# Optimization experiments

Hardware: AMD Instinct MI355X
Metric: run time of the kernel (lower is better)

## Reference

```python
import jax, jax.numpy as jnp
import numpy as np

B, T, C = 2, 8192, 1024
H, BS, LW = 16, 64, 128          # num_heads, block_size, local_window_size
D = C // H                        # head_dim = 64
W = BS + LW                       # max window length per block = 192
NB = T // BS                      # number of blocks


def setup_inputs() -> dict:
    key = jax.random.key(0)
    ks = jax.random.split(key, 11)
    s = 1.0 / np.sqrt(C)          # small init so softmax is not saturated
    return {
        'query': jax.random.normal(ks[0], (B, T, C), jnp.float32),
        'key':   jax.random.normal(ks[1], (B, T, C), jnp.float32),
        'value': jax.random.normal(ks[2], (B, T, C), jnp.float32),
        'Wq': jax.random.normal(ks[3], (C, C), jnp.float32) * s,
        'bq': jax.random.normal(ks[4], (C,), jnp.float32) * s,
        'Wk': jax.random.normal(ks[5], (C, C), jnp.float32) * s,
        'bk': jax.random.normal(ks[6], (C,), jnp.float32) * s,
        'Wv': jax.random.normal(ks[7], (C, C), jnp.float32) * s,
        'bv': jax.random.normal(ks[8], (C,), jnp.float32) * s,
        'Wo': jax.random.normal(ks[9], (C, C), jnp.float32) * s,
        'bo': jax.random.normal(ks[10], (C,), jnp.float32) * s,
    }


def reference(query, key, value, Wq, bq, Wk, bk, Wv, bv, Wo, bo):
    # projections -> (B, H, T, D)
    def proj(x, Wt, bt):
        return (x @ Wt.T + bt).reshape(B, T, H, D).transpose(0, 2, 1, 3)

    scale = jnp.asarray(D, query.dtype) ** -0.5
    q = proj(query, Wq, bq) * scale
    k = proj(key, Wk, bk)
    v = proj(value, Wv, bv)

    # per-block window indices: block i attends to [i - LW//2, i + BS + LW//2)
    starts = jnp.arange(NB) * BS                              # (NB,)
    idx = starts[:, None] + jnp.arange(-LW // 2, BS + LW // 2)  # (NB, W)
    valid = (idx >= 0) & (idx < T)                            # (NB, W)
    cidx = jnp.clip(idx, 0, T - 1)

    q_blk = q.reshape(B, H, NB, BS, D)
    k_win = k[:, :, cidx, :]                                  # (B, H, NB, W, D)
    v_win = v[:, :, cidx, :]

    scores = jnp.einsum('bhnqd,bhnkd->bhnqk', q_blk, k_win).astype(jnp.float32)
    scores = jnp.where(valid[None, None, :, None, :], scores, -jnp.inf)
    probs = jax.nn.softmax(scores, axis=-1).astype(q.dtype)

    out = jnp.einsum('bhnqk,bhnkd->bhnqd', probs, v_win)      # (B, H, NB, BS, D)
    out = out.reshape(B, H, T, D).transpose(0, 2, 1, 3).reshape(B, T, C)
    return out @ Wo.T + bo
```

## Files before the change

### kernel.cpp

```cpp
#include <hip/hip_runtime.h>
#include <hip/hip_bf16.h>
#include <type_traits>

#define BATCH 2
#define SEQ   8192
#define CH    1024
#define NH    16
#define BLK   64
#define WIN   192
#define NBL   128
#define DH    64
#define MR    (BATCH*SEQ)

typedef __bf16 bf16x8 __attribute__((ext_vector_type(8)));
typedef float  f32x4  __attribute__((ext_vector_type(4)));

__device__ __forceinline__ f32x4 zero4() {
    f32x4 z; z[0]=0.f; z[1]=0.f; z[2]=0.f; z[3]=0.f; return z;
}

union Pack8 { __hip_bfloat16 h[8]; uint4 u; };

typedef const __attribute__((address_space(1))) unsigned int* gas_ptr;
typedef       __attribute__((address_space(3))) unsigned int* las_ptr;

__device__ __forceinline__ void gload_lds16(const __hip_bfloat16* g, __hip_bfloat16* l) {
    __builtin_amdgcn_global_load_lds((gas_ptr)(const void*)g, (las_ptr)(void*)l, 16, 0, 0);
}

__device__ __forceinline__ int xcd_swz(int bid, int nwg) {
    return (bid & 7) * (nwg >> 3) + (bid >> 3);
}

__global__ __launch_bounds__(256) void pack_bf16(
    const float* __restrict__ src, __hip_bfloat16* __restrict__ dst, int n8)
{
    int i = blockIdx.x * 256 + threadIdx.x;
    if (i >= n8) return;
    const float4* s = reinterpret_cast<const float4*>(src);
    float4 a = s[2 * i], b = s[2 * i + 1];
    Pack8 p;
    p.h[0] = __float2bfloat16(a.x); p.h[1] = __float2bfloat16(a.y);
    p.h[2] = __float2bfloat16(a.z); p.h[3] = __float2bfloat16(a.w);
    p.h[4] = __float2bfloat16(b.x); p.h[5] = __float2bfloat16(b.y);
    p.h[6] = __float2bfloat16(b.z); p.h[7] = __float2bfloat16(b.w);
    reinterpret_cast<uint4*>(dst)[i] = p.u;
}


__device__ __forceinline__ void stage_half(
    const __hip_bfloat16* __restrict__ g, int goff,
    __hip_bfloat16* sm, int loff, int tid)
{
    gload_lds16(g + goff,            sm + loff + tid * 8);
    gload_lds16(g + goff + 128 * CH, sm + loff + (tid + 512) * 8);
}

#define SB0 __builtin_amdgcn_sched_barrier(0)
#define LGKM0 do { asm volatile("s_waitcnt lgkmcnt(0)" ::: "memory"); \
                   __builtin_amdgcn_sched_barrier(0); } while (0)
#define VMCNT(n) do { asm volatile("s_waitcnt vmcnt(" #n ")" ::: "memory"); \
                      __builtin_amdgcn_sched_barrier(0); } while (0)

template<int MH, bool RB>
__device__ __forceinline__ void phase_reads(
    const __hip_bfloat16* Ak, const __hip_bfloat16* Bk,
    int aoff, int boff, bf16x8 (&af)[4], bf16x8 (&bfk)[4])
{
    if constexpr (RB) {
        #pragma unroll
        for (int j = 0; j < 4; ++j)
            bfk[j] = *reinterpret_cast<const bf16x8*>(Bk + boff + j * 512);
    }
    #pragma unroll
    for (int i = 0; i < 4; ++i)
        af[i] = *reinterpret_cast<const bf16x8*>(Ak + aoff + (MH * 4 + i) * 512);
}

template<int MH>
__device__ __forceinline__ void phase_mfma16(
    const bf16x8 (&af)[4], const bf16x8 (&bfk)[4], f32x4 (&acc)[8][4])
{
    __builtin_amdgcn_s_setprio(1);
    #pragma unroll
    for (int i = 0; i < 4; ++i)
        #pragma unroll
        for (int j = 0; j < 4; ++j)
            acc[MH * 4 + i][j] = __builtin_amdgcn_mfma_f32_16x16x32_bf16(
                af[i], bfk[j], acc[MH * 4 + i][j], 0, 0, 0);
    __builtin_amdgcn_s_setprio(0);
}

template<typename OT>
__device__ __forceinline__ void gemm_body256(
    const __hip_bfloat16* __restrict__ A, const __hip_bfloat16* __restrict__ Wb,
    const float* __restrict__ bias, OT* __restrict__ out, float alpha,
    int m0, int n0, __hip_bfloat16* sm)
{
    const int tid  = threadIdx.x;
    const int wid  = tid >> 6;
    const int lane = tid & 63;
    const int quad = lane >> 4;
    const int l16  = lane & 15;
    const int wr   = wid >> 2, wc = wid & 3;

    const int r0 = tid >> 2;
    const int s0 = (tid & 3) ^ ((tid >> 3) & 3);
    const int offA0 = (m0 + r0) * CH + s0 * 8;
    const int offB0 = (n0 + r0) * CH + s0 * 8;

    const int cq   = quad ^ ((l16 >> 1) & 3);
    const int aoff = ((wr * 128 + l16) * 4 + cq) * 8;
    const int boff = ((wc * 64  + l16) * 4 + cq) * 8;

    f32x4 acc[8][4];
    #pragma unroll
    for (int i = 0; i < 8; ++i)
        #pragma unroll
        for (int j = 0; j < 4; ++j) acc[i][j] = zero4();

    stage_half(A,  offA0,      sm, 0,             tid);
    stage_half(Wb, offB0,      sm, 32768,         tid);
    stage_half(A,  offA0 + 32, sm, 8192,          tid);
    stage_half(Wb, offB0 + 32, sm, 32768 + 8192,  tid);
    VMCNT(4);
    __builtin_amdgcn_s_barrier();
    SB0;

    bf16x8 af[4], bfk[4];

    #pragma unroll 1
    for (int t = 0; t < 15; ++t) {
        const int cur = t & 1, nb = cur ^ 1;
        const int kn  = (t + 1) * 64;
        const __hip_bfloat16* As_ = sm + cur * 16384;
        const __hip_bfloat16* Bs_ = sm + 32768 + cur * 16384;

        phase_reads<0, true>(As_, Bs_, aoff, boff, af, bfk);
        stage_half(A, offA0 + kn, sm, nb * 16384, tid);
        SB0;
        __builtin_amdgcn_s_barrier();
        LGKM0;
        phase_mfma16<0>(af, bfk, acc);
        __builtin_amdgcn_s_barrier();

        phase_reads<1, false>(As_, Bs_, aoff, boff, af, bfk);
        stage_half(Wb, offB0 + kn, sm, 32768 + nb * 16384, tid);
        SB0;
        __builtin_amdgcn_s_barrier();
        LGKM0;
        phase_mfma16<1>(af, bfk, acc);
        VMCNT(4);
        __builtin_amdgcn_s_barrier();

        phase_reads<0, true>(As_ + 8192, Bs_ + 8192, aoff, boff, af, bfk);
        stage_half(A, offA0 + kn + 32, sm, nb * 16384 + 8192, tid);
        SB0;
        __builtin_amdgcn_s_barrier();
        LGKM0;
        phase_mfma16<0>(af, bfk, acc);
        __builtin_amdgcn_s_barrier();

        phase_reads<1, false>(As_ + 8192, Bs_ + 8192, aoff, boff, af, bfk);
        stage_half(Wb, offB0 + kn + 32, sm, 32768 + nb * 16384 + 8192, tid);
        SB0;
        __builtin_amdgcn_s_barrier();
        LGKM0;
        phase_mfma16<1>(af, bfk, acc);
        VMCNT(4);
        __builtin_amdgcn_s_barrier();
    }

    {
        const __hip_bfloat16* As_ = sm + 16384;
        const __hip_bfloat16* Bs_ = sm + 32768 + 16384;

        phase_reads<0, true>(As_, Bs_, aoff, boff, af, bfk);
        SB0;
        __builtin_amdgcn_s_barrier();
        LGKM0;
        phase_mfma16<0>(af, bfk, acc);
        __builtin_amdgcn_s_barrier();

        phase_reads<1, false>(As_, Bs_, aoff, boff, af, bfk);
        SB0;
        __builtin_amdgcn_s_barrier();
        LGKM0;
        phase_mfma16<1>(af, bfk, acc);
        VMCNT(0);
        __builtin_amdgcn_s_barrier();

        phase_reads<0, true>(As_ + 8192, Bs_ + 8192, aoff, boff, af, bfk);
        SB0;
        __builtin_amdgcn_s_barrier();
        LGKM0;
        phase_mfma16<0>(af, bfk, acc);
        __builtin_amdgcn_s_barrier();

        phase_reads<1, false>(As_ + 8192, Bs_ + 8192, aoff, boff, af, bfk);
        SB0;
        __builtin_amdgcn_s_barrier();
        LGKM0;
        phase_mfma16<1>(af, bfk, acc);
    }

    #pragma unroll
    for (int j = 0; j < 4; ++j) {
        const int col = n0 + wc * 64 + j * 16 + l16;
        const float bv = bias[col];
        #pragma unroll
        for (int i = 0; i < 8; ++i) {
            #pragma unroll
            for (int r = 0; r < 4; ++r) {
                const int row = m0 + wr * 128 + i * 16 + quad * 4 + r;
                float v = alpha * (acc[i][j][r] + bv);
                if constexpr (std::is_same<OT, float>::value)
                    out[(size_t)row * CH + col] = v;
                else
                    out[(size_t)row * CH + col] = __float2bfloat16(v);
            }
        }
    }
}

__device__ __forceinline__ void gemm_tile256(int& m0, int& n0) {
    int bid = blockIdx.y * 4 + blockIdx.x;
    int swz = (bid & 7) * 32 + (bid >> 3);
    m0 = (swz >> 2) * 256;
    n0 = (swz & 3) * 256;
}

__global__ __launch_bounds__(512, 2) void gemm_qk256(
    const __hip_bfloat16* __restrict__ A0, const __hip_bfloat16* __restrict__ W0,
    const float* __restrict__ b0, __hip_bfloat16* __restrict__ o0, float alpha0,
    const __hip_bfloat16* __restrict__ A1, const __hip_bfloat16* __restrict__ W1,
    const float* __restrict__ b1, __hip_bfloat16* __restrict__ o1)
{
    __shared__ alignas(16) __hip_bfloat16 sm[65536];
    int m0, n0; gemm_tile256(m0, n0);
    if (blockIdx.z == 0)
        gemm_body256<__hip_bfloat16>(A0, W0, b0, o0, alpha0, m0, n0, sm);
    else
        gemm_body256<__hip_bfloat16>(A1, W1, b1, o1, 1.0f, m0, n0, sm);
}

template<typename OT>
__global__ __launch_bounds__(512, 2) void gemm_one256(
    const __hip_bfloat16* __restrict__ A, const __hip_bfloat16* __restrict__ Wb,
    const float* __restrict__ bias, OT* __restrict__ out)
{
    __shared__ alignas(16) __hip_bfloat16 sm[65536];
    int m0, n0; gemm_tile256(m0, n0);
    gemm_body256<OT>(A, Wb, bias, out, 1.0f, m0, n0, sm);
}

__global__ __launch_bounds__(256) void attn_kernel(
    const __hip_bfloat16* __restrict__ qg,
    const __hip_bfloat16* __restrict__ kg,
    const __hip_bfloat16* __restrict__ vg,
    __hip_bfloat16* __restrict__ ctx)
{
    __shared__ alignas(16) char smem[62464];
    auto qs = reinterpret_cast<__hip_bfloat16(*)[72]>(smem);
    auto ks = reinterpret_cast<__hip_bfloat16(*)[72]>(smem + 9216);
    auto vt = reinterpret_cast<__hip_bfloat16(*)[200]>(smem + 36864);
    auto ps = reinterpret_cast<__hip_bfloat16(*)[200]>(smem);

    const int blk = xcd_swz(blockIdx.x, BATCH * NH * NBL);
    const int n = blk & (NBL - 1);
    const int h = (blk >> 7) & (NH - 1);
    const int b = blk >> 11;
    const int t0  = n * BLK;
    const int kst = t0 - 64;
    const int tid = threadIdx.x;
    const size_t baseBH = (size_t)b * SEQ * CH + (size_t)h * DH;

    #pragma unroll
    for (int it = 0; it < 2; it++) {
        int c = tid + it * 256;
        int row = c >> 3, seg = c & 7;
        *reinterpret_cast<uint4*>(&qs[row][seg * 8]) =
            *reinterpret_cast<const uint4*>(qg + baseBH + (size_t)(t0 + row) * CH + seg * 8);
    }
    #pragma unroll
    for (int it = 0; it < 6; it++) {
        int c = tid + it * 256;
        int row = c >> 3, seg = c & 7;
        int tr = kst + row; tr = tr < 0 ? 0 : (tr >= SEQ ? SEQ - 1 : tr);
        *reinterpret_cast<uint4*>(&ks[row][seg * 8]) =
            *reinterpret_cast<const uint4*>(kg + baseBH + (size_t)tr * CH + seg * 8);
    }
    #pragma unroll
    for (int it = 0; it < 6; it++) {
        int c = tid + it * 256;
        int j = c % WIN, seg = c / WIN;
        int tr = kst + j; tr = tr < 0 ? 0 : (tr >= SEQ ? SEQ - 1 : tr);
        Pack8 p;
        p.u = *reinterpret_cast<const uint4*>(vg + baseBH + (size_t)tr * CH + seg * 8);
        #pragma unroll
        for (int e = 0; e < 8; e++) vt[seg * 8 + e][j] = p.h[e];
    }
    __syncthreads();

    const int wid = tid >> 6, lane = tid & 63, quad = lane >> 4, l16 = lane & 15;

    f32x4 sc[12];
    #pragma unroll
    for (int j = 0; j < 12; j++) sc[j] = zero4();
    #pragma unroll
    for (int kk = 0; kk < 2; kk++) {
        bf16x8 aq = *reinterpret_cast<const bf16x8*>(&qs[wid * 16 + l16][kk * 32 + quad * 8]);
        #pragma unroll
        for (int j = 0; j < 12; j++) {
            bf16x8 bk = *reinterpret_cast<const bf16x8*>(&ks[j * 16 + l16][kk * 32 + quad * 8]);
            sc[j] = __builtin_amdgcn_mfma_f32_16x16x32_bf16(aq, bk, sc[j], 0, 0, 0);
        }
    }
    __syncthreads();

    #pragma unroll
    for (int r = 0; r < 4; r++) {
        float s[12];
        float mx = -3.0e38f;
        #pragma unroll
        for (int j = 0; j < 12; j++) {
            int col = j * 16 + l16;
            int tr = kst + col;
            bool valid = (tr >= 0) && (tr < SEQ);
            s[j] = valid ? sc[j][r] : -3.0e38f;
            mx = fmaxf(mx, s[j]);
        }
        #pragma unroll
        for (int o = 1; o < 16; o <<= 1) mx = fmaxf(mx, __shfl_xor(mx, o, 64));
        float sum = 0.f;
        #pragma unroll
        for (int j = 0; j < 12; j++) {
            float e = __expf(s[j] - mx);
            s[j] = e;
            sum += e;
        }
        #pragma unroll
        for (int o = 1; o < 16; o <<= 1) sum += __shfl_xor(sum, o, 64);
        const float inv = 1.f / sum;
        const int row = wid * 16 + quad * 4 + r;
        #pragma unroll
        for (int j = 0; j < 12; j++)
            ps[row][j * 16 + l16] = __float2bfloat16(s[j] * inv);
    }
    __syncthreads();

    f32x4 oa[4];
    #pragma unroll
    for (int j = 0; j < 4; j++) oa[j] = zero4();
    #pragma unroll
    for (int kk = 0; kk < 6; kk++) {
        bf16x8 ap = *reinterpret_cast<const bf16x8*>(&ps[wid * 16 + l16][kk * 32 + quad * 8]);
        #pragma unroll
        for (int j = 0; j < 4; j++) {
            bf16x8 bv = *reinterpret_cast<const bf16x8*>(&vt[j * 16 + l16][kk * 32 + quad * 8]);
            oa[j] = __builtin_amdgcn_mfma_f32_16x16x32_bf16(ap, bv, oa[j], 0, 0, 0);
        }
    }
    #pragma unroll
    for (int j = 0; j < 4; j++) {
        const int d = j * 16 + l16;
        #pragma unroll
        for (int r = 0; r < 4; r++) {
            const int i = wid * 16 + quad * 4 + r;
            ctx[baseBH + (size_t)(t0 + i) * CH + d] = __float2bfloat16(oa[j][r]);
        }
    }
}

extern "C" void kernel_launch(void* const* d_in, const int* in_sizes, int n_in,
                              void* d_out, int out_size, void* d_ws, size_t ws_size,
                              hipStream_t stream)
{
    const float* query = (const float*)d_in[0];
    const float* key_i = (const float*)d_in[1];
    const float* value = (const float*)d_in[2];
    const float* Wq = (const float*)d_in[3];
    const float* bq = (const float*)d_in[4];
    const float* Wk = (const float*)d_in[5];
    const float* bk = (const float*)d_in[6];
    const float* Wv = (const float*)d_in[7];
    const float* bv = (const float*)d_in[8];
    const float* Wo = (const float*)d_in[9];
    const float* bo = (const float*)d_in[10];
    float* out = (float*)d_out;

    const size_t NELEM = (size_t)MR * CH;
    const size_t WELEM = (size_t)CH * CH;

    __hip_bfloat16* S0 = (__hip_bfloat16*)d_ws;
    __hip_bfloat16* S1 = S0 + NELEM;
    __hip_bfloat16* S2 = S1 + NELEM;
    __hip_bfloat16* S3 = S2 + NELEM;
    __hip_bfloat16* wqb = S3;
    __hip_bfloat16* wkb = S3 + WELEM;
    __hip_bfloat16* wvb = S3 + 2 * WELEM;
    __hip_bfloat16* wob = S3 + 3 * WELEM;

    __hip_bfloat16* xq = (__hip_bfloat16*)d_out;
    __hip_bfloat16* xk = xq + NELEM;
    __hip_bfloat16* vb = (__hip_bfloat16*)d_out;
    __hip_bfloat16* qb = S1;
    __hip_bfloat16* kb = S2;
    __hip_bfloat16* cb = S0;

    const int nA8 = (int)(NELEM / 8);
    const int nW8 = (int)(WELEM / 8);

    pack_bf16<<<nA8 / 256, 256, 0, stream>>>(query, xq, nA8);
    pack_bf16<<<nA8 / 256, 256, 0, stream>>>(key_i, xk, nA8);
    pack_bf16<<<nA8 / 256, 256, 0, stream>>>(value, S0, nA8);
    pack_bf16<<<nW8 / 256, 256, 0, stream>>>(Wq, wqb, nW8);
    pack_bf16<<<nW8 / 256, 256, 0, stream>>>(Wk, wkb, nW8);
    pack_bf16<<<nW8 / 256, 256, 0, stream>>>(Wv, wvb, nW8);
    pack_bf16<<<nW8 / 256, 256, 0, stream>>>(Wo, wob, nW8);

    dim3 ggrid(CH / 256, MR / 256);
    dim3 qkgrid(CH / 256, MR / 256, 2);

    gemm_qk256<<<qkgrid, 512, 0, stream>>>(xq, wqb, bq, qb, 0.125f,
                                           xk, wkb, bk, kb);
    gemm_one256<__hip_bfloat16><<<ggrid, 512, 0, stream>>>(S0, wvb, bv, vb);

    attn_kernel<<<BATCH * NH * NBL, 256, 0, stream>>>(qb, kb, vb, cb);

    gemm_one256<float><<<ggrid, 512, 0, stream>>>(cb, wob, bo, out);
}
```

Measured before the change: 448.8 us.

## Fuse bf16 pack launches and load attention Q directly into registers

Replaces seven separate fp32-to-bf16 pack launches with one pack_all kernel that routes each block to its source tensor by block index, removing launch overhead and tail gaps between the launches. In the attention kernel, Q fragments now go straight from global memory into MFMA operand registers instead of through LDS. This shrinks shared memory from about 61 KB to 52 KB, and the launch bound is raised to request 3 blocks per CU. The risks are uncoalesced per-lane Q loads and register pressure from the occupancy hint.

```diff
diff --git a/kernel.cpp b/kernel.cpp
--- a/kernel.cpp
+++ b/kernel.cpp
@@ -32,11 +32,33 @@
     return (bid & 7) * (nwg >> 3) + (bid >> 3);
 }
 
-__global__ __launch_bounds__(256) void pack_bf16(
-    const float* __restrict__ src, __hip_bfloat16* __restrict__ dst, int n8)
-{
-    int i = blockIdx.x * 256 + threadIdx.x;
-    if (i >= n8) return;
+__global__ __launch_bounds__(256) void pack_all(
+    const float* __restrict__ q,  const float* __restrict__ k,
+    const float* __restrict__ v,
+    const float* __restrict__ wq, const float* __restrict__ wk,
+    const float* __restrict__ wv, const float* __restrict__ wo,
+    __hip_bfloat16* __restrict__ xq, __hip_bfloat16* __restrict__ xk,
+    __hip_bfloat16* __restrict__ xv,
+    __hip_bfloat16* __restrict__ wqb, __hip_bfloat16* __restrict__ wkb,
+    __hip_bfloat16* __restrict__ wvb, __hip_bfloat16* __restrict__ wob)
+{
+    const int NA8B = (MR * CH / 8) / 256;
+    const int NW8B = (CH * CH / 8) / 256;
+    int bid = blockIdx.x;
+    const float* src;
+    __hip_bfloat16* dst;
+    int rel;
+    if (bid < 3 * NA8B) {
+        int t = bid / NA8B; rel = bid - t * NA8B;
+        src = (t == 0) ? q : (t == 1) ? k : v;
+        dst = (t == 0) ? xq : (t == 1) ? xk : xv;
+    } else {
+        int b2 = bid - 3 * NA8B;
+        int t = b2 / NW8B; rel = b2 - t * NW8B;
+        src = (t == 0) ? wq : (t == 1) ? wk : (t == 2) ? wv : wo;
+        dst = (t == 0) ? wqb : (t == 1) ? wkb : (t == 2) ? wvb : wob;
+    }
+    int i = rel * 256 + threadIdx.x;
     const float4* s = reinterpret_cast<const float4*>(src);
     float4 a = s[2 * i], b = s[2 * i + 1];
     Pack8 p;
@@ -254,16 +276,15 @@
     gemm_body256<OT>(A, Wb, bias, out, 1.0f, m0, n0, sm);
 }
 
-__global__ __launch_bounds__(256) void attn_kernel(
+__global__ __launch_bounds__(256, 3) void attn_kernel(
     const __hip_bfloat16* __restrict__ qg,
     const __hip_bfloat16* __restrict__ kg,
     const __hip_bfloat16* __restrict__ vg,
     __hip_bfloat16* __restrict__ ctx)
 {
-    __shared__ alignas(16) char smem[62464];
-    auto qs = reinterpret_cast<__hip_bfloat16(*)[72]>(smem);
-    auto ks = reinterpret_cast<__hip_bfloat16(*)[72]>(smem + 9216);
-    auto vt = reinterpret_cast<__hip_bfloat16(*)[200]>(smem + 36864);
+    __shared__ alignas(16) char smem[53248];
+    auto ks = reinterpret_cast<__hip_bfloat16(*)[72]>(smem);
+    auto vt = reinterpret_cast<__hip_bfloat16(*)[200]>(smem + 27648);
     auto ps = reinterpret_cast<__hip_bfloat16(*)[200]>(smem);
 
     const int blk = xcd_swz(blockIdx.x, BATCH * NH * NBL);
@@ -275,13 +296,12 @@
     const int tid = threadIdx.x;
     const size_t baseBH = (size_t)b * SEQ * CH + (size_t)h * DH;
 
-    #pragma unroll
-    for (int it = 0; it < 2; it++) {
-        int c = tid + it * 256;
-        int row = c >> 3, seg = c & 7;
-        *reinterpret_cast<uint4*>(&qs[row][seg * 8]) =
-            *reinterpret_cast<const uint4*>(qg + baseBH + (size_t)(t0 + row) * CH + seg * 8);
-    }
+    const int wid = tid >> 6, lane = tid & 63, quad = lane >> 4, l16 = lane & 15;
+
+    const __hip_bfloat16* qrow = qg + baseBH + (size_t)(t0 + wid * 16 + l16) * CH + quad * 8;
+    bf16x8 aq0 = *reinterpret_cast<const bf16x8*>(qrow);
+    bf16x8 aq1 = *reinterpret_cast<const bf16x8*>(qrow + 32);
+
     #pragma unroll
     for (int it = 0; it < 6; it++) {
         int c = tid + it * 256;
@@ -302,19 +322,15 @@
     }
     __syncthreads();
 
-    const int wid = tid >> 6, lane = tid & 63, quad = lane >> 4, l16 = lane & 15;
-
     f32x4 sc[12];
     #pragma unroll
     for (int j = 0; j < 12; j++) sc[j] = zero4();
     #pragma unroll
-    for (int kk = 0; kk < 2; kk++) {
-        bf16x8 aq = *reinterpret_cast<const bf16x8*>(&qs[wid * 16 + l16][kk * 32 + quad * 8]);
-        #pragma unroll
-        for (int j = 0; j < 12; j++) {
-            bf16x8 bk = *reinterpret_cast<const bf16x8*>(&ks[j * 16 + l16][kk * 32 + quad * 8]);
-            sc[j] = __builtin_amdgcn_mfma_f32_16x16x32_bf16(aq, bk, sc[j], 0, 0, 0);
-        }
+    for (int j = 0; j < 12; j++) {
+        bf16x8 bk0 = *reinterpret_cast<const bf16x8*>(&ks[j * 16 + l16][quad * 8]);
+        sc[j] = __builtin_amdgcn_mfma_f32_16x16x32_bf16(aq0, bk0, sc[j], 0, 0, 0);
+        bf16x8 bk1 = *reinterpret_cast<const bf16x8*>(&ks[j * 16 + l16][32 + quad * 8]);
+        sc[j] = __builtin_amdgcn_mfma_f32_16x16x32_bf16(aq1, bk1, sc[j], 0, 0, 0);
     }
     __syncthreads();
 
@@ -408,16 +424,12 @@
     __hip_bfloat16* kb = S2;
     __hip_bfloat16* cb = S0;
 
-    const int nA8 = (int)(NELEM / 8);
-    const int nW8 = (int)(WELEM / 8);
-
-    pack_bf16<<<nA8 / 256, 256, 0, stream>>>(query, xq, nA8);
-    pack_bf16<<<nA8 / 256, 256, 0, stream>>>(key_i, xk, nA8);
-    pack_bf16<<<nA8 / 256, 256, 0, stream>>>(value, S0, nA8);
-    pack_bf16<<<nW8 / 256, 256, 0, stream>>>(Wq, wqb, nW8);
-    pack_bf16<<<nW8 / 256, 256, 0, stream>>>(Wk, wkb, nW8);
-    pack_bf16<<<nW8 / 256, 256, 0, stream>>>(Wv, wvb, nW8);
-    pack_bf16<<<nW8 / 256, 256, 0, stream>>>(Wo, wob, nW8);
+    const int NA8B = (int)((NELEM / 8) / 256);
+    const int NW8B = (int)((WELEM / 8) / 256);
+
+    pack_all<<<3 * NA8B + 4 * NW8B, 256, 0, stream>>>(
+        query, key_i, value, Wq, Wk, Wv, Wo,
+        xq, xk, S0, wqb, wkb, wvb, wob);
 
     dim3 ggrid(CH / 256, MR / 256);
     dim3 qkgrid(CH / 256, MR / 256, 2);
```

Result: faster. 428.1 us (-4.6%).
